# Optimization experiments

Measured on AMD Instinct MI355X. Metric: run time of the kernel, lower is better.

The kernel has to match this reference:

```python
import jax, jax.numpy as jnp
import numpy as np

B, CIN, COUT, COFF, H, W = 4, 256, 256, 256, 64, 64
DG, K = 16, 3            # deformable groups, kernel size
KK = K * K               # 9 taps


def _conv3x3(x, w, b):
    y = jax.lax.conv_general_dilated(x, w, window_strides=(1, 1), padding='SAME',
                                     dimension_numbers=('NCHW', 'OIHW', 'NCHW'))
    return y + b[None, :, None, None]


def _bilinear_sample(xg, ys, xs):
    # xg: [B,DG,Cg,H,W]; ys,xs: [B,DG,Ho,Wo] float sampling coords (zero padding outside)
    Bn, dg, Cg, Hh, Ww = xg.shape
    xf = xg.reshape(Bn, dg, Cg, Hh * Ww)
    y0 = jnp.floor(ys)
    x0 = jnp.floor(xs)
    wy = (ys - y0)[:, :, None]  # [B,DG,1,Ho,Wo]
    wx = (xs - x0)[:, :, None]

    def gather(yi, xi):
        valid = (yi >= 0) & (yi < Hh) & (xi >= 0) & (xi < Ww)
        yc = jnp.clip(yi, 0, Hh - 1).astype(jnp.int32)
        xc = jnp.clip(xi, 0, Ww - 1).astype(jnp.int32)
        idx = (yc * Ww + xc).reshape(Bn, dg, 1, -1)
        v = jnp.take_along_axis(xf, jnp.broadcast_to(idx, (Bn, dg, Cg, idx.shape[-1])), axis=-1)
        v = v.reshape(Bn, dg, Cg, ys.shape[2], ys.shape[3])
        return v * valid[:, :, None].astype(xg.dtype)

    v00 = gather(y0, x0)
    v01 = gather(y0, x0 + 1)
    v10 = gather(y0 + 1, x0)
    v11 = gather(y0 + 1, x0 + 1)
    return v00 * (1 - wy) * (1 - wx) + v01 * (1 - wy) * wx + v10 * wy * (1 - wx) + v11 * wy * wx


def _deform_conv2d(x, offset, mask, weight, bias):
    # torchvision modulated deform_conv2d, stride=1, padding=1, dilation=1, groups=1
    Bn, C, Hh, Ww = x.shape
    Cg = C // DG
    xg = x.reshape(Bn, DG, Cg, Hh, Ww)
    # offset channel layout: 2*(g*KK + k) -> dy, +1 -> dx
    off = offset.reshape(Bn, DG, KK, 2, Hh, Ww)
    msk = mask.reshape(Bn, DG, KK, Hh, Ww)
    wk = weight.reshape(weight.shape[0], DG, Cg, K, K)
    hb = jnp.arange(Hh, dtype=x.dtype)[:, None]
    wb = jnp.arange(Ww, dtype=x.dtype)[None, :]
    acc = jnp.zeros((Bn, weight.shape[0], Hh, Ww), dtype=x.dtype)
    for ki in range(K):
        for kj in range(K):
            k = ki * K + kj
            ys = hb - 1 + ki + off[:, :, k, 0]   # padding=1, dilation=1
            xs = wb - 1 + kj + off[:, :, k, 1]
            s = _bilinear_sample(xg, ys, xs) * msk[:, :, k][:, :, None]  # [B,DG,Cg,H,W]
            acc = acc + jnp.einsum('bgchw,ogc->bohw', s, wk[:, :, :, ki, kj])
    return acc + bias[None, :, None, None]


def setup_inputs() -> dict:
    key = jax.random.key(0)
    ks = jax.random.split(key, 10)
    s = 0.02
    return {
        'x': jax.random.normal(ks[0], (B, CIN, H, W), jnp.float32),
        'offset_feat': jax.random.normal(ks[1], (B, COFF, H, W), jnp.float32),
        'weight': jax.random.normal(ks[2], (COUT, CIN, K, K), jnp.float32) * s,
        'bias': jax.random.normal(ks[3], (COUT,), jnp.float32) * s,
        'w1': jax.random.normal(ks[4], (COUT, COFF, K, K), jnp.float32) * s,
        'b1': jax.random.normal(ks[5], (COUT,), jnp.float32) * s,
        'w2': jax.random.normal(ks[6], (COUT, COUT, K, K), jnp.float32) * s,
        'b2': jax.random.normal(ks[7], (COUT,), jnp.float32) * s,
        'w3': jax.random.normal(ks[8], (27 * DG, COUT, K, K), jnp.float32) * 0.01,
        'b3': jax.random.normal(ks[9], (27 * DG,), jnp.float32) * 0.01,
    }


def reference(x, offset_feat, weight, bias, w1, b1, w2, b2, w3, b3):
    out = jax.nn.silu(_conv3x3(offset_feat, w1, b1))
    out = jax.nn.silu(_conv3x3(out, w2, b2))
    out = _conv3x3(out, w3, b3)                 # [B, 27*DG, H, W]
    o1, o2, m = jnp.split(out, 3, axis=1)
    offset = jnp.concatenate([o1, o2], axis=1)  # [B, 2*DG*9, H, W]
    mask = jax.nn.sigmoid(m)                    # [B, DG*9, H, W]
    return _deform_conv2d(x, offset, mask, weight, bias)
```

## Files before the change

kernel.cpp:

```cpp
#include <hip/hip_runtime.h>
#include <math.h>

typedef __attribute__((ext_vector_type(8))) short  bf16x8;
typedef __attribute__((ext_vector_type(8))) unsigned short u16x8;
typedef __attribute__((ext_vector_type(4))) float  f32x4;

__device__ __forceinline__ float b2f(unsigned short h) {
  return __uint_as_float(((unsigned int)h) << 16);
}
__device__ __forceinline__ unsigned short f2bf(float f) {
  unsigned int u = __float_as_uint(f);
  unsigned int r = (u + 0x7fffu + ((u >> 16) & 1u)) >> 16;
  return (unsigned short)r;
}
__device__ __forceinline__ void gload16(const unsigned short* g, unsigned short* l) {
  __builtin_amdgcn_global_load_lds(
      (const __attribute__((address_space(1))) void*)g,
      (__attribute__((address_space(3))) void*)l, 16, 0, 0);
}

__global__ __launch_bounds__(256) void nhwc_kernel(const float* __restrict__ in,
                                                   unsigned short* __restrict__ out) {
  const int y = blockIdx.x, b = blockIdx.y;
  const int t = threadIdx.x;
  __shared__ float lds[64 * 65];
  for (int c0 = 0; c0 < 256; c0 += 64) {
    #pragma unroll
    for (int i = 0; i < 16; ++i) {
      int cl = i * 4 + (t >> 6);
      int xx = t & 63;
      lds[cl * 65 + xx] = in[(((size_t)b * 256 + c0 + cl) * 64 + y) * 64 + xx];
    }
    __syncthreads();
    #pragma unroll
    for (int i = 0; i < 16; ++i) {
      int xx = i * 4 + (t >> 6);
      int cl = t & 63;
      out[(((size_t)b * 64 + y) * 64 + xx) * 256 + c0 + cl] = f2bf(lds[cl * 65 + xx]);
    }
    __syncthreads();
  }
}

__global__ __launch_bounds__(256) void wprep_kernel(const float* __restrict__ w,
                                                    unsigned short* __restrict__ Wp,
                                                    int COUT_valid) {
  const int kk = blockIdx.x;
  const int co = blockIdx.y;
  const int ci = threadIdx.x;
  float v = (co < COUT_valid) ? w[((size_t)co * 256 + ci) * 9 + kk] : 0.0f;
  Wp[(size_t)co * 2304 + kk * 256 + ci] = f2bf(v);
}

__global__ __launch_bounds__(256) void sampler_kernel(const float* __restrict__ t3,
                                                      const unsigned short* __restrict__ xh,
                                                      unsigned short* __restrict__ S) {
  const int t = threadIdx.x;
  const int g = t & 15;
  const int m = blockIdx.x * 16 + (t >> 4);
  const int b = m >> 12, pix = m & 4095, y = pix >> 6, x = pix & 63;
  const float* off = t3 + (size_t)m * 432;

  #pragma unroll
  for (int kk = 0; kk < 9; ++kk) {
    const int ki = kk / 3, kj = kk % 3;
    float dyv = off[2 * (g * 9 + kk)];
    float dxv = off[2 * (g * 9 + kk) + 1];
    float ml  = off[288 + g * 9 + kk];
    float mk  = 1.0f / (1.0f + __expf(-ml));
    float ysf = (float)(y - 1 + ki) + dyv;
    float xsf = (float)(x - 1 + kj) + dxv;
    float y0f = floorf(ysf), x0f = floorf(xsf);
    float wy = ysf - y0f, wx = xsf - x0f;
    int yi0 = (int)y0f, xi0 = (int)x0f;
    int yi1 = yi0 + 1, xi1 = xi0 + 1;
    bool vy0 = (yi0 >= 0) && (yi0 < 64), vy1 = (yi1 >= 0) && (yi1 < 64);
    bool vx0 = (xi0 >= 0) && (xi0 < 64), vx1 = (xi1 >= 0) && (xi1 < 64);
    int yc0 = min(max(yi0, 0), 63), yc1 = min(max(yi1, 0), 63);
    int xc0 = min(max(xi0, 0), 63), xc1 = min(max(xi1, 0), 63);
    float w00 = (vy0 && vx0) ? (1.f - wy) * (1.f - wx) * mk : 0.f;
    float w01 = (vy0 && vx1) ? (1.f - wy) * wx * mk : 0.f;
    float w10 = (vy1 && vx0) ? wy * (1.f - wx) * mk : 0.f;
    float w11 = (vy1 && vx1) ? wy * wx * mk : 0.f;

    float sacc[16];
    #pragma unroll
    for (int c = 0; c < 16; ++c) sacc[c] = 0.f;

    const size_t bbase = (size_t)(b << 12) * 256 + g * 16;
    const int p00 = yc0 * 64 + xc0, p01 = yc0 * 64 + xc1;
    const int p10 = yc1 * 64 + xc0, p11 = yc1 * 64 + xc1;
    {
      u16x8 lo = *(const u16x8*)(xh + bbase + (size_t)p00 * 256);
      u16x8 hi = *(const u16x8*)(xh + bbase + (size_t)p00 * 256 + 8);
      #pragma unroll
      for (int j = 0; j < 8; ++j) { sacc[j] += w00 * b2f(lo[j]); sacc[8 + j] += w00 * b2f(hi[j]); }
    }
    {
      u16x8 lo = *(const u16x8*)(xh + bbase + (size_t)p01 * 256);
      u16x8 hi = *(const u16x8*)(xh + bbase + (size_t)p01 * 256 + 8);
      #pragma unroll
      for (int j = 0; j < 8; ++j) { sacc[j] += w01 * b2f(lo[j]); sacc[8 + j] += w01 * b2f(hi[j]); }
    }
    {
      u16x8 lo = *(const u16x8*)(xh + bbase + (size_t)p10 * 256);
      u16x8 hi = *(const u16x8*)(xh + bbase + (size_t)p10 * 256 + 8);
      #pragma unroll
      for (int j = 0; j < 8; ++j) { sacc[j] += w10 * b2f(lo[j]); sacc[8 + j] += w10 * b2f(hi[j]); }
    }
    {
      u16x8 lo = *(const u16x8*)(xh + bbase + (size_t)p11 * 256);
      u16x8 hi = *(const u16x8*)(xh + bbase + (size_t)p11 * 256 + 8);
      #pragma unroll
      for (int j = 0; j < 8; ++j) { sacc[j] += w11 * b2f(lo[j]); sacc[8 + j] += w11 * b2f(hi[j]); }
    }
    u16x8 olo, ohi;
    #pragma unroll
    for (int j = 0; j < 8; ++j) { olo[j] = f2bf(sacc[j]); ohi[j] = f2bf(sacc[8 + j]); }
    unsigned short* sp = S + (size_t)m * 2304 + kk * 256 + g * 16;
    *(u16x8*)sp = olo;
    *(u16x8*)(sp + 8) = ohi;
  }
}

template<int EPI, bool IMPLICIT>
__global__ __launch_bounds__(256, 2) void gemm_kernel(
    const unsigned short* __restrict__ A,
    const unsigned short* __restrict__ W,
    const float* __restrict__ bias,
    void* __restrict__ outp,
    const unsigned short* __restrict__ zbuf,
    int K, int Nvalid) {
  constexpr int BM = 128, BN = 128, BK = 64;
  constexpr int NSTEP = 36;
  constexpr int BUFE = (BM + BN) * BK;
  __shared__ unsigned short lds[2][BUFE];

  const int t = threadIdx.x, lane = t & 63, w = t >> 6;
  const int wm = w >> 1, wn = w & 1;
  const int m0 = blockIdx.x * BM, n0 = blockIdx.y * BN;

  const unsigned short* baseA[4];
  const unsigned short* zsrcA[4];
  unsigned int vmaskA[4];
  #pragma unroll
  for (int i = 0; i < 4; ++i) {
    int c   = (i * 4 + w) * 64 + lane;
    int row = c >> 3;
    int ccl = (c & 7) ^ (row & 7);
    int m   = m0 + row;
    if (IMPLICIT) {
      int y = (m >> 6) & 63, x = m & 63;
      unsigned int vm = 0;
      #pragma unroll
      for (int kk = 0; kk < 9; ++kk) {
        int dy = kk / 3 - 1, dx = kk % 3 - 1;
        if ((unsigned)(y + dy) < 64u && (unsigned)(x + dx) < 64u) vm |= (1u << kk);
      }
      vmaskA[i] = vm;
      baseA[i] = A + (size_t)m * 256 + ccl * 8;
      zsrcA[i] = zbuf + ccl * 8;
    } else {
      baseA[i] = A + (size_t)m * K + ccl * 8;
      zsrcA[i] = zbuf;
      vmaskA[i] = 0;
    }
  }
  const unsigned short* baseB[4];
  #pragma unroll
  for (int j = 0; j < 4; ++j) {
    int c   = (j * 4 + w) * 64 + lane;
    int row = c >> 3;
    int ccl = (c & 7) ^ (row & 7);
    baseB[j] = W + (size_t)(n0 + row) * K + ccl * 8;
  }

  int offA[4][2], offB[4][2];
  #pragma unroll
  for (int mi = 0; mi < 4; ++mi) {
    int r = wm * 64 + mi * 16 + (lane & 15);
    #pragma unroll
    for (int kh = 0; kh < 2; ++kh) {
      int ccl = kh * 4 + (lane >> 4);
      offA[mi][kh] = r * 64 + ((ccl ^ (r & 7)) * 8);
    }
  }
  #pragma unroll
  for (int nj = 0; nj < 4; ++nj) {
    int r = wn * 64 + nj * 16 + (lane & 15);
    #pragma unroll
    for (int kh = 0; kh < 2; ++kh) {
      int ccl = kh * 4 + (lane >> 4);
      offB[nj][kh] = BM * BK + r * 64 + ((ccl ^ (r & 7)) * 8);
    }
  }

  f32x4 acc[4][4];
  #pragma unroll
  for (int mi = 0; mi < 4; ++mi)
    #pragma unroll
    for (int nj = 0; nj < 4; ++nj) acc[mi][nj] = (f32x4){0.f, 0.f, 0.f, 0.f};

  auto STAGE = [&](int sn, unsigned short* buf) {
    if (IMPLICIT) {
      int kkn = sn >> 2;
      int ci0 = (sn & 3) * 64;
      int q3  = kkn / 3;
      int soff = ((q3 - 1) * 64 + (kkn - q3 * 3 - 1)) * 256 + ci0;
      #pragma unroll
      for (int i = 0; i < 4; ++i) {
        const unsigned short* src = ((vmaskA[i] >> kkn) & 1u) ? baseA[i] + soff : zsrcA[i];
        gload16(src, buf + (i * 4 + w) * 512);
      }
    } else {
      #pragma unroll
      for (int i = 0; i < 4; ++i)
        gload16(baseA[i] + (size_t)sn * 64, buf + (i * 4 + w) * 512);
    }
    #pragma unroll
    for (int j = 0; j < 4; ++j)
      gload16(baseB[j] + (size_t)sn * 64, buf + BM * BK + (j * 4 + w) * 512);
  };

  STAGE(0, lds[0]);

  for (int s = 0; s < NSTEP; ++s) {
    if (s + 1 < NSTEP) {
      STAGE(s + 1, lds[(s + 1) & 1]);
      asm volatile("s_waitcnt vmcnt(8)" ::: "memory");
    } else {
      asm volatile("s_waitcnt vmcnt(0)" ::: "memory");
    }
    __builtin_amdgcn_s_barrier();
    __builtin_amdgcn_sched_barrier(0);

    const unsigned short* cb = lds[s & 1];
    bf16x8 af[4][2], bfg[4][2];
    #pragma unroll
    for (int mi = 0; mi < 4; ++mi)
      #pragma unroll
      for (int kh = 0; kh < 2; ++kh)
        af[mi][kh] = *(const bf16x8*)&cb[offA[mi][kh]];
    #pragma unroll
    for (int nj = 0; nj < 4; ++nj)
      #pragma unroll
      for (int kh = 0; kh < 2; ++kh)
        bfg[nj][kh] = *(const bf16x8*)&cb[offB[nj][kh]];

    #pragma unroll
    for (int kh = 0; kh < 2; ++kh)
      #pragma unroll
      for (int mi = 0; mi < 4; ++mi)
        #pragma unroll
        for (int nj = 0; nj < 4; ++nj)
          acc[mi][nj] = __builtin_amdgcn_mfma_f32_16x16x32_bf16(af[mi][kh], bfg[nj][kh],
                                                                acc[mi][nj], 0, 0, 0);
    __builtin_amdgcn_sched_barrier(0);
    asm volatile("s_waitcnt lgkmcnt(0)" ::: "memory");
    __builtin_amdgcn_s_barrier();
  }

  const int gmBase = m0 + wm * 64 + (lane >> 4) * 4;
  const int gnBase = n0 + wn * 64 + (lane & 15);
  #pragma unroll
  for (int nj = 0; nj < 4; ++nj) {
    const int gn = gnBase + nj * 16;
    const float bv = (gn < Nvalid) ? bias[gn] : 0.f;
    #pragma unroll
    for (int mi = 0; mi < 4; ++mi) {
      #pragma unroll
      for (int r = 0; r < 4; ++r) {
        const int gm = gmBase + mi * 16 + r;
        float v = acc[mi][nj][r] + bv;
        if (EPI == 0) {
          float sv = v / (1.0f + __expf(-v));
          ((unsigned short*)outp)[(size_t)gm * 256 + gn] = f2bf(sv);
        } else if (EPI == 1) {
          if (gn < Nvalid) ((float*)outp)[(size_t)gm * 432 + gn] = v;
        } else {
          ((float*)outp)[((size_t)(gm >> 12) * 256 + gn) * 4096 + (gm & 4095)] = v;
        }
      }
    }
  }
}

extern "C" void kernel_launch(void* const* d_in, const int* in_sizes, int n_in,
                              void* d_out, int out_size, void* d_ws, size_t ws_size,
                              hipStream_t stream) {
  const float* x      = (const float*)d_in[0];
  const float* offeat = (const float*)d_in[1];
  const float* weight = (const float*)d_in[2];
  const float* bias   = (const float*)d_in[3];
  const float* w1     = (const float*)d_in[4];
  const float* b1     = (const float*)d_in[5];
  const float* w2     = (const float*)d_in[6];
  const float* b2     = (const float*)d_in[7];
  const float* w3     = (const float*)d_in[8];
  const float* b3     = (const float*)d_in[9];
  float* out = (float*)d_out;

  char* ws = (char*)d_ws;
  unsigned short* xh  = (unsigned short*)(ws + 0);
  float*          t3  = (float*)(ws + 8388608);
  unsigned short* Wd  = (unsigned short*)(ws + 36700160);
  unsigned short* zb  = (unsigned short*)(ws + 37879808);
  unsigned short* S   = (unsigned short*)(ws + 37880064);
  unsigned short* fh  = (unsigned short*)(ws + 37880064);
  unsigned short* t1  = (unsigned short*)(ws + 46268672);
  unsigned short* t2  = (unsigned short*)(ws + 54657280);
  unsigned short* W1p = (unsigned short*)(ws + 63045888);
  unsigned short* W2p = (unsigned short*)(ws + 64225536);
  unsigned short* W3p = (unsigned short*)(ws + 65405184);

  hipMemsetAsync(zb, 0, 256, stream);

  nhwc_kernel<<<dim3(64, 4), 256, 0, stream>>>(x, xh);
  nhwc_kernel<<<dim3(64, 4), 256, 0, stream>>>(offeat, fh);
  wprep_kernel<<<dim3(9, 256), 256, 0, stream>>>(w1, W1p, 256);
  wprep_kernel<<<dim3(9, 256), 256, 0, stream>>>(w2, W2p, 256);
  wprep_kernel<<<dim3(9, 512), 256, 0, stream>>>(w3, W3p, 432);
  wprep_kernel<<<dim3(9, 256), 256, 0, stream>>>(weight, Wd, 256);

  gemm_kernel<0, true><<<dim3(128, 2), 256, 0, stream>>>(fh, W1p, b1, t1, zb, 2304, 256);
  gemm_kernel<0, true><<<dim3(128, 2), 256, 0, stream>>>(t1, W2p, b2, t2, zb, 2304, 256);
  gemm_kernel<1, true><<<dim3(128, 4), 256, 0, stream>>>(t2, W3p, b3, t3, zb, 2304, 432);

  sampler_kernel<<<dim3(1024), 256, 0, stream>>>(t3, xh, S);
  gemm_kernel<2, false><<<dim3(128, 2), 256, 0, stream>>>(S, Wd, bias, out, zb, 2304, 256);
}
```

Before: 211.3 us.

## Store activations and weights in K-chunk-major planes of 64 channels

```diff
diff --git a/kernel.cpp b/kernel.cpp
--- a/kernel.cpp
+++ b/kernel.cpp
@@ -4,6 +4,8 @@
 typedef __attribute__((ext_vector_type(8))) short  bf16x8;
 typedef __attribute__((ext_vector_type(8))) unsigned short u16x8;
 typedef __attribute__((ext_vector_type(4))) float  f32x4;
+
+#define MTOT 16384
 
 __device__ __forceinline__ float b2f(unsigned short h) {
   return __uint_as_float(((unsigned int)h) << 16);
@@ -32,11 +34,13 @@
       lds[cl * 65 + xx] = in[(((size_t)b * 256 + c0 + cl) * 64 + y) * 64 + xx];
     }
     __syncthreads();
+    const int plane = c0 >> 6;
     #pragma unroll
     for (int i = 0; i < 16; ++i) {
       int xx = i * 4 + (t >> 6);
       int cl = t & 63;
-      out[(((size_t)b * 64 + y) * 64 + xx) * 256 + c0 + cl] = f2bf(lds[cl * 65 + xx]);
+      int m  = (b << 12) + (y << 6) + xx;
+      out[((size_t)plane * MTOT + m) * 64 + cl] = f2bf(lds[cl * 65 + xx]);
     }
     __syncthreads();
   }
@@ -44,12 +48,13 @@
 
 __global__ __launch_bounds__(256) void wprep_kernel(const float* __restrict__ w,
                                                     unsigned short* __restrict__ Wp,
-                                                    int COUT_valid) {
-  const int kk = blockIdx.x;
-  const int co = blockIdx.y;
-  const int ci = threadIdx.x;
-  float v = (co < COUT_valid) ? w[((size_t)co * 256 + ci) * 9 + kk] : 0.0f;
-  Wp[(size_t)co * 2304 + kk * 256 + ci] = f2bf(v);
+                                                    int NPAD, int COUT_valid) {
+  const int kkc4 = blockIdx.x;
+  const int kk = kkc4 >> 2, c4 = kkc4 & 3;
+  const int co = blockIdx.y * 4 + (threadIdx.x >> 6);
+  const int c16 = threadIdx.x & 63;
+  float v = (co < COUT_valid) ? w[((size_t)co * 256 + c4 * 64 + c16) * 9 + kk] : 0.0f;
+  Wp[((size_t)kkc4 * NPAD + co) * 64 + c16] = f2bf(v);
 }
 
 __global__ __launch_bounds__(256) void sampler_kernel(const float* __restrict__ t3,
@@ -60,6 +65,7 @@
   const int m = blockIdx.x * 16 + (t >> 4);
   const int b = m >> 12, pix = m & 4095, y = pix >> 6, x = pix & 63;
   const float* off = t3 + (size_t)m * 432;
+  const size_t gbase = ((size_t)(g >> 2) * MTOT + ((size_t)b << 12)) * 64 + (g & 3) * 16;
 
   #pragma unroll
   for (int kk = 0; kk < 9; ++kk) {
@@ -87,50 +93,49 @@
     #pragma unroll
     for (int c = 0; c < 16; ++c) sacc[c] = 0.f;
 
-    const size_t bbase = (size_t)(b << 12) * 256 + g * 16;
     const int p00 = yc0 * 64 + xc0, p01 = yc0 * 64 + xc1;
     const int p10 = yc1 * 64 + xc0, p11 = yc1 * 64 + xc1;
     {
-      u16x8 lo = *(const u16x8*)(xh + bbase + (size_t)p00 * 256);
-      u16x8 hi = *(const u16x8*)(xh + bbase + (size_t)p00 * 256 + 8);
+      u16x8 lo = *(const u16x8*)(xh + gbase + (size_t)p00 * 64);
+      u16x8 hi = *(const u16x8*)(xh + gbase + (size_t)p00 * 64 + 8);
       #pragma unroll
       for (int j = 0; j < 8; ++j) { sacc[j] += w00 * b2f(lo[j]); sacc[8 + j] += w00 * b2f(hi[j]); }
     }
     {
-      u16x8 lo = *(const u16x8*)(xh + bbase + (size_t)p01 * 256);
-      u16x8 hi = *(const u16x8*)(xh + bbase + (size_t)p01 * 256 + 8);
+      u16x8 lo = *(const u16x8*)(xh + gbase + (size_t)p01 * 64);
+      u16x8 hi = *(const u16x8*)(xh + gbase + (size_t)p01 * 64 + 8);
       #pragma unroll
       for (int j = 0; j < 8; ++j) { sacc[j] += w01 * b2f(lo[j]); sacc[8 + j] += w01 * b2f(hi[j]); }
     }
     {
-      u16x8 lo = *(const u16x8*)(xh + bbase + (size_t)p10 * 256);
-      u16x8 hi = *(const u16x8*)(xh + bbase + (size_t)p10 * 256 + 8);
+      u16x8 lo = *(const u16x8*)(xh + gbase + (size_t)p10 * 64);
+      u16x8 hi = *(const u16x8*)(xh + gbase + (size_t)p10 * 64 + 8);
       #pragma unroll
       for (int j = 0; j < 8; ++j) { sacc[j] += w10 * b2f(lo[j]); sacc[8 + j] += w10 * b2f(hi[j]); }
     }
     {
-      u16x8 lo = *(const u16x8*)(xh + bbase + (size_t)p11 * 256);
-      u16x8 hi = *(const u16x8*)(xh + bbase + (size_t)p11 * 256 + 8);
+      u16x8 lo = *(const u16x8*)(xh + gbase + (size_t)p11 * 64);
+      u16x8 hi = *(const u16x8*)(xh + gbase + (size_t)p11 * 64 + 8);
       #pragma unroll
       for (int j = 0; j < 8; ++j) { sacc[j] += w11 * b2f(lo[j]); sacc[8 + j] += w11 * b2f(hi[j]); }
     }
     u16x8 olo, ohi;
     #pragma unroll
     for (int j = 0; j < 8; ++j) { olo[j] = f2bf(sacc[j]); ohi[j] = f2bf(sacc[8 + j]); }
-    unsigned short* sp = S + (size_t)m * 2304 + kk * 256 + g * 16;
+    unsigned short* sp = S + ((size_t)(kk * 4 + (g >> 2)) * MTOT + m) * 64 + (g & 3) * 16;
     *(u16x8*)sp = olo;
     *(u16x8*)(sp + 8) = ohi;
   }
 }
 
-template<int EPI, bool IMPLICIT>
+template<int NPAD, int EPI, bool IMPLICIT>
 __global__ __launch_bounds__(256, 2) void gemm_kernel(
     const unsigned short* __restrict__ A,
     const unsigned short* __restrict__ W,
     const float* __restrict__ bias,
     void* __restrict__ outp,
     const unsigned short* __restrict__ zbuf,
-    int K, int Nvalid) {
+    int Nvalid) {
   constexpr int BM = 128, BN = 128, BK = 64;
   constexpr int NSTEP = 36;
   constexpr int BUFE = (BM + BN) * BK;
@@ -149,6 +154,8 @@
     int row = c >> 3;
     int ccl = (c & 7) ^ (row & 7);
     int m   = m0 + row;
+    baseA[i] = A + (size_t)m * 64 + ccl * 8;
+    zsrcA[i] = zbuf + ccl * 8;
     if (IMPLICIT) {
       int y = (m >> 6) & 63, x = m & 63;
       unsigned int vm = 0;
@@ -158,11 +165,7 @@
         if ((unsigned)(y + dy) < 64u && (unsigned)(x + dx) < 64u) vm |= (1u << kk);
       }
       vmaskA[i] = vm;
-      baseA[i] = A + (size_t)m * 256 + ccl * 8;
-      zsrcA[i] = zbuf + ccl * 8;
     } else {
-      baseA[i] = A + (size_t)m * K + ccl * 8;
-      zsrcA[i] = zbuf;
       vmaskA[i] = 0;
     }
   }
@@ -172,7 +175,7 @@
     int c   = (j * 4 + w) * 64 + lane;
     int row = c >> 3;
     int ccl = (c & 7) ^ (row & 7);
-    baseB[j] = W + (size_t)(n0 + row) * K + ccl * 8;
+    baseB[j] = W + (size_t)(n0 + row) * 64 + ccl * 8;
   }
 
   int offA[4][2], offB[4][2];
@@ -202,24 +205,26 @@
     for (int nj = 0; nj < 4; ++nj) acc[mi][nj] = (f32x4){0.f, 0.f, 0.f, 0.f};
 
   auto STAGE = [&](int sn, unsigned short* buf) {
+    const long boff = (long)sn * (NPAD * 64);
     if (IMPLICIT) {
       int kkn = sn >> 2;
-      int ci0 = (sn & 3) * 64;
       int q3  = kkn / 3;
-      int soff = ((q3 - 1) * 64 + (kkn - q3 * 3 - 1)) * 256 + ci0;
+      int dy = q3 - 1, dx = kkn - q3 * 3 - 1;
+      const long aoff = (long)(sn & 3) * (MTOT * 64) + (long)(dy * 64 + dx) * 64;
       #pragma unroll
       for (int i = 0; i < 4; ++i) {
-        const unsigned short* src = ((vmaskA[i] >> kkn) & 1u) ? baseA[i] + soff : zsrcA[i];
+        const unsigned short* src = ((vmaskA[i] >> kkn) & 1u) ? baseA[i] + aoff : zsrcA[i];
         gload16(src, buf + (i * 4 + w) * 512);
       }
     } else {
+      const long aoff = (long)sn * (MTOT * 64);
       #pragma unroll
       for (int i = 0; i < 4; ++i)
-        gload16(baseA[i] + (size_t)sn * 64, buf + (i * 4 + w) * 512);
+        gload16(baseA[i] + aoff, buf + (i * 4 + w) * 512);
     }
     #pragma unroll
     for (int j = 0; j < 4; ++j)
-      gload16(baseB[j] + (size_t)sn * 64, buf + BM * BK + (j * 4 + w) * 512);
+      gload16(baseB[j] + boff, buf + BM * BK + (j * 4 + w) * 512);
   };
 
   STAGE(0, lds[0]);
@@ -274,7 +279,7 @@
         float v = acc[mi][nj][r] + bv;
         if (EPI == 0) {
           float sv = v / (1.0f + __expf(-v));
-          ((unsigned short*)outp)[(size_t)gm * 256 + gn] = f2bf(sv);
+          ((unsigned short*)outp)[((size_t)(gn >> 6) * MTOT + gm) * 64 + (gn & 63)] = f2bf(sv);
         } else if (EPI == 1) {
           if (gn < Nvalid) ((float*)outp)[(size_t)gm * 432 + gn] = v;
         } else {
@@ -317,15 +322,15 @@
 
   nhwc_kernel<<<dim3(64, 4), 256, 0, stream>>>(x, xh);
   nhwc_kernel<<<dim3(64, 4), 256, 0, stream>>>(offeat, fh);
-  wprep_kernel<<<dim3(9, 256), 256, 0, stream>>>(w1, W1p, 256);
-  wprep_kernel<<<dim3(9, 256), 256, 0, stream>>>(w2, W2p, 256);
-  wprep_kernel<<<dim3(9, 512), 256, 0, stream>>>(w3, W3p, 432);
-  wprep_kernel<<<dim3(9, 256), 256, 0, stream>>>(weight, Wd, 256);
-
-  gemm_kernel<0, true><<<dim3(128, 2), 256, 0, stream>>>(fh, W1p, b1, t1, zb, 2304, 256);
-  gemm_kernel<0, true><<<dim3(128, 2), 256, 0, stream>>>(t1, W2p, b2, t2, zb, 2304, 256);
-  gemm_kernel<1, true><<<dim3(128, 4), 256, 0, stream>>>(t2, W3p, b3, t3, zb, 2304, 432);
+  wprep_kernel<<<dim3(36, 64), 256, 0, stream>>>(w1, W1p, 256, 256);
+  wprep_kernel<<<dim3(36, 64), 256, 0, stream>>>(w2, W2p, 256, 256);
+  wprep_kernel<<<dim3(36, 128), 256, 0, stream>>>(w3, W3p, 512, 432);
+  wprep_kernel<<<dim3(36, 64), 256, 0, stream>>>(weight, Wd, 256, 256);
+
+  gemm_kernel<256, 0, true><<<dim3(128, 2), 256, 0, stream>>>(fh, W1p, b1, t1, zb, 256);
+  gemm_kernel<256, 0, true><<<dim3(128, 2), 256, 0, stream>>>(t1, W2p, b2, t2, zb, 256);
+  gemm_kernel<512, 1, true><<<dim3(128, 4), 256, 0, stream>>>(t2, W3p, b3, t3, zb, 432);
 
   sampler_kernel<<<dim3(1024), 256, 0, stream>>>(t3, xh, S);
-  gemm_kernel<2, false><<<dim3(128, 2), 256, 0, stream>>>(S, Wd, bias, out, zb, 2304, 256);
-}
+  gemm_kernel<256, 2, false><<<dim3(128, 2), 256, 0, stream>>>(S, Wd, bias, out, zb, 256);
+}
```

After: 201.0 us. 4.9% less time.
